# Performance work log

Measured on AMD Instinct MI355X. Metric: run time of the kernel, lower is better.

The kernel has to match this reference:

```python
import jax, jax.numpy as jnp
import numpy as np

B, S, D, H = 2, 2048, 1024, 16
HD = D // H  # head_dim = 64

def setup_inputs() -> dict:
    key = jax.random.key(0)
    ks = jax.random.split(key, 10)
    s = 1.0 / np.sqrt(D)
    return {
        "hidden_states": jax.random.normal(ks[0], (B, S, D), jnp.float32),
        "attention_mask": jnp.ones((B, S), jnp.float32),
        "q_w": jax.random.uniform(ks[1], (D, D), jnp.float32, -s, s),
        "q_b": jax.random.uniform(ks[2], (D,), jnp.float32, -s, s),
        "k_w": jax.random.uniform(ks[3], (D, D), jnp.float32, -s, s),
        "k_b": jax.random.uniform(ks[4], (D,), jnp.float32, -s, s),
        "v_w": jax.random.uniform(ks[5], (D, D), jnp.float32, -s, s),
        "v_b": jax.random.uniform(ks[6], (D,), jnp.float32, -s, s),
        "o_w": jax.random.uniform(ks[7], (D, D), jnp.float32, -s, s),
        "o_b": jax.random.uniform(ks[8], (D,), jnp.float32, -s, s),
    }

def reference(hidden_states, attention_mask, q_w, q_b, k_w, k_b, v_w, v_b, o_w, o_b):
    scale = HD ** -0.5
    # projections; torch Linear: x @ W^T + b. Here weights stored as (D, D) used directly.
    q = hidden_states @ q_w + q_b  # [B,S,D]
    k = hidden_states @ k_w + k_b
    v = hidden_states @ v_w + v_b
    # split heads -> [B,H,S,HD]
    q = q.reshape(B, S, H, HD).transpose(0, 2, 1, 3)
    k = k.reshape(B, S, H, HD).transpose(0, 2, 1, 3)
    v = v.reshape(B, S, H, HD).transpose(0, 2, 1, 3)
    scores = jnp.einsum('bhqd,bhkd->bhqk', q, k) * scale  # [B,H,S,S]
    # additive mask from 2D [B,S] mask (1=keep, 0=mask)
    scores = scores + (1.0 - attention_mask)[:, None, None, :] * -10000.0
    attn = jax.nn.softmax(scores, axis=-1)
    ctx = jnp.einsum('bhqk,bhkd->bhqd', attn, v)  # [B,H,S,HD]
    ctx = ctx.transpose(0, 2, 1, 3).reshape(B, S, D)
    return ctx @ o_w + o_b
```

## Files before the change

kernel.cpp:

```cpp
#include <hip/hip_runtime.h>
#include <hip/hip_bf16.h>

#define B_ 2
#define S_ 2048
#define D_ 1024
#define H_ 16
#define HD_ 64

#define QSCALE 0.18033688f
#define MLOG2E 14426.950408f

#define EXP2(x) __builtin_amdgcn_exp2f(x)

typedef __attribute__((ext_vector_type(8))) short bf16x8;
typedef __attribute__((ext_vector_type(4))) short short4v;
typedef __attribute__((ext_vector_type(4))) float floatx4;
typedef __attribute__((ext_vector_type(16))) float f32x16;

static __device__ __forceinline__ short f2bf(float f) {
  union { float f; unsigned int i; } c; c.f = f;
  unsigned int r = c.i + 0x7FFFu + ((c.i >> 16) & 1u);
  return (short)(r >> 16);
}

static __device__ __forceinline__ int cvtpk_bf16(float a, float b) {
  int r;
  asm("v_cvt_pk_bf16_f32 %0, %1, %2" : "=v"(r) : "v"(a), "v"(b));
  return r;
}
static __device__ __forceinline__ void swap32(int& a, int& b) {
  asm("v_permlane32_swap_b32 %0, %1" : "+v"(a), "+v"(b));
}

static __device__ __forceinline__ void gld_lds16(const void* g, void* l) {
  __builtin_amdgcn_global_load_lds(
      (const __attribute__((address_space(1))) unsigned int*)g,
      (__attribute__((address_space(3))) unsigned int*)l, 16, 0, 0);
}

__global__ __launch_bounds__(256)
void prep(const float* __restrict__ w0, const float* __restrict__ w1,
          const float* __restrict__ w2, const float* __restrict__ w3,
          const float* __restrict__ hs, short* __restrict__ WT,
          short* __restrict__ Xb) {
  const int z = blockIdx.z;
  if (z < 4) {
    __shared__ short t[64][65];
    const float* src = z == 0 ? w0 : z == 1 ? w1 : z == 2 ? w2 : w3;
    short* dst = WT + (size_t)z * D_ * D_;
    const int tx = threadIdx.x & 63, ty = threadIdx.x >> 6;
    const int r0 = blockIdx.y * 64, c0 = blockIdx.x * 64;
    for (int r = ty; r < 64; r += 4)
      t[r][tx] = f2bf(src[(size_t)(r0 + r) * D_ + c0 + tx]);
    __syncthreads();
    for (int r = ty; r < 64; r += 4)
      dst[(size_t)(c0 + r) * D_ + r0 + tx] = t[tx][r];
  } else {
    const int bid = blockIdx.y * 16 + blockIdx.x;
    const float4* in4 = (const float4*)hs;
    short4v* out4 = (short4v*)Xb;
#pragma unroll
    for (int i = 0; i < 16; i++) {
      const int idx = bid * 4096 + i * 256 + threadIdx.x;
      const float4 v = in4[idx];
      short4v o;
      o[0] = f2bf(v.x); o[1] = f2bf(v.y); o[2] = f2bf(v.z); o[3] = f2bf(v.w);
      out4[idx] = o;
    }
  }
}

__global__ __launch_bounds__(256, 2)
void gemm_qkv(const short* __restrict__ X, const short* __restrict__ WT,
              const float* __restrict__ qb, const float* __restrict__ kb,
              const float* __restrict__ vb,
              short* __restrict__ Qo, short* __restrict__ Ko,
              short* __restrict__ Vt) {
  __shared__ __align__(16) short As[128 * 32];
  __shared__ __align__(16) short Bs[128 * 32];
  const int tid = threadIdx.x;
  const int wave = tid >> 6, lane = tid & 63;
  const int col = lane & 15, quad = lane >> 4;
  const int m0 = blockIdx.x * 128;
  const int nt = blockIdx.y;
  const int widx = nt >> 3;
  const int n1 = (nt & 7) * 128;
  const short* Bsrc = WT + (size_t)widx * D_ * D_ + (size_t)n1 * D_;
  const int b = m0 >> 11;

  const int srow = tid >> 2;
  const int skcol = (tid & 3) * 8;
  const short* ga = X + (size_t)(m0 + srow) * D_ + skcol;
  const short* gb = Bsrc + (size_t)srow * D_ + skcol;
  short* la = As + tid * 8;
  short* lb = Bs + tid * 8;

  floatx4 acc[4][4];
#pragma unroll
  for (int i = 0; i < 4; i++)
#pragma unroll
    for (int j = 0; j < 4; j++) acc[i][j] = floatx4{0.f, 0.f, 0.f, 0.f};

  if (widx < 2) {
    const int wseq = (wave >> 1) * 64;
    const int wfeat = (wave & 1) * 64;
    for (int k0 = 0; k0 < D_; k0 += 32) {
      gld_lds16(ga, la);
      gld_lds16(ga + 64 * D_, la + 2048);
      gld_lds16(gb, lb);
      gld_lds16(gb + 64 * D_, lb + 2048);
      ga += 32; gb += 32;
      __syncthreads();
      bf16x8 xf[4], wf[4];
#pragma unroll
      for (int j = 0; j < 4; j++)
        xf[j] = *(const bf16x8*)(As + (wseq + j * 16 + col) * 32 + quad * 8);
#pragma unroll
      for (int i = 0; i < 4; i++)
        wf[i] = *(const bf16x8*)(Bs + (wfeat + i * 16 + col) * 32 + quad * 8);
#pragma unroll
      for (int i = 0; i < 4; i++)
#pragma unroll
        for (int j = 0; j < 4; j++)
          acc[i][j] = __builtin_amdgcn_mfma_f32_16x16x32_bf16(wf[i], xf[j],
                                                              acc[i][j], 0, 0, 0);
      __syncthreads();
    }
    const float* bias = widx == 0 ? qb : kb;
    short* dst = widx == 0 ? Qo : Ko;
    const float scale = widx == 0 ? QSCALE : 1.0f;
#pragma unroll
    for (int i = 0; i < 4; i++) {
      const int nf = n1 + wfeat + i * 16 + quad * 4;
      const int h = nf >> 6, hd = nf & 63;
      const float4 bv = *(const float4*)(bias + nf);
#pragma unroll
      for (int j = 0; j < 4; j++) {
        const int s = (m0 + wseq + j * 16 + col) & (S_ - 1);
        short4v pk;
        pk[0] = f2bf((acc[i][j][0] + bv.x) * scale);
        pk[1] = f2bf((acc[i][j][1] + bv.y) * scale);
        pk[2] = f2bf((acc[i][j][2] + bv.z) * scale);
        pk[3] = f2bf((acc[i][j][3] + bv.w) * scale);
        *(short4v*)(dst + ((size_t)(b * H_ + h) * S_ + s) * HD_ + hd) = pk;
      }
    }
  } else {
    const int wrow = (wave & 1) * 64;
    const int wcol = (wave >> 1) * 64;
    for (int k0 = 0; k0 < D_; k0 += 32) {
      gld_lds16(ga, la);
      gld_lds16(ga + 64 * D_, la + 2048);
      gld_lds16(gb, lb);
      gld_lds16(gb + 64 * D_, lb + 2048);
      ga += 32; gb += 32;
      __syncthreads();
      bf16x8 af[4], bfr[4];
#pragma unroll
      for (int i = 0; i < 4; i++)
        af[i] = *(const bf16x8*)(As + (wrow + i * 16 + col) * 32 + quad * 8);
#pragma unroll
      for (int j = 0; j < 4; j++)
        bfr[j] = *(const bf16x8*)(Bs + (wcol + j * 16 + col) * 32 + quad * 8);
#pragma unroll
      for (int i = 0; i < 4; i++)
#pragma unroll
        for (int j = 0; j < 4; j++)
          acc[i][j] = __builtin_amdgcn_mfma_f32_16x16x32_bf16(af[i], bfr[j],
                                                              acc[i][j], 0, 0, 0);
      __syncthreads();
    }
    float bv[4];
#pragma unroll
    for (int j = 0; j < 4; j++) bv[j] = vb[n1 + wcol + j * 16 + col];
#pragma unroll
    for (int i = 0; i < 4; i++) {
      const int s = (m0 + wrow + i * 16 + quad * 4) & (S_ - 1);
#pragma unroll
      for (int j = 0; j < 4; j++) {
        const int nl = n1 + wcol + j * 16 + col;
        const int h = nl >> 6, hd = nl & 63;
        short4v pk;
#pragma unroll
        for (int r = 0; r < 4; r++) pk[r] = f2bf(acc[i][j][r] + bv[j]);
        *(short4v*)(Vt + ((size_t)(b * H_ + h) * HD_ + hd) * S_ + s) = pk;
      }
    }
  }
}

__global__ __launch_bounds__(256, 2)
void attn(const short* __restrict__ Q, const short* __restrict__ K,
          const short* __restrict__ Vt, const float* __restrict__ mask,
          short* __restrict__ ctx) {
  __shared__ __align__(16) short Ks[2][8192];
  __shared__ __align__(16) short Vs[2][8192];
  __shared__ __align__(16) float Wb[S_];
  const int tid = threadIdx.x, wave = tid >> 6, lane = tid & 63;
  const int l31 = lane & 31, hi = lane >> 5, x7 = l31 & 7;
  const int lin = blockIdx.x;
  const int qt = (lin >> 3) & 15;
  const int gi = (lin & 7) + ((lin >> 7) << 3);
  const int h = gi & 15, b = gi >> 4;
  const short* Qh = Q + (size_t)(b * H_ + h) * S_ * HD_;
  const short* Kh = K + (size_t)(b * H_ + h) * S_ * HD_;
  const short* Vh = Vt + (size_t)(b * H_ + h) * HD_ * S_;
  const float* mk = mask + (size_t)b * S_;
  const int q0 = qt * 128 + wave * 32;

  int srow[4], schk[4], sts[4];
#pragma unroll
  for (int i = 0; i < 4; i++) {
    const int s = tid + i * 256;
    sts[i] = s >> 9;
    const int s9 = s & 511;
    srow[i] = s9 >> 3;
    schk[i] = ((s9 & 7) ^ (srow[i] & 7)) * 8;
  }

#pragma unroll
  for (int i = 0; i < 4; i++) {
    gld_lds16(Kh + (size_t)(sts[i] * 64 + srow[i]) * HD_ + schk[i],
              &Ks[0][(tid + i * 256) * 8]);
    gld_lds16(Vh + (size_t)srow[i] * S_ + sts[i] * 64 + schk[i],
              &Vs[0][(tid + i * 256) * 8]);
  }

  for (int i = tid; i < S_; i += 256)
    Wb[i] = (mk[i] - 1.0f) * MLOG2E;

  bf16x8 qf[4];
  {
    const short* qp = Qh + (size_t)(q0 + l31) * HD_ + hi * 8;
#pragma unroll
    for (int c = 0; c < 4; c++) qf[c] = *(const bf16x8*)(qp + c * 16);
  }

  bf16x8 ones;
#pragma unroll
  for (int i = 0; i < 8; i++) ones[i] = (short)0x3F80;

  f32x16 acc0, acc1, rsa;
#pragma unroll
  for (int r = 0; r < 16; r++) { acc0[r] = 0.f; acc1[r] = 0.f; rsa[r] = 0.f; }

  const int kbase = l31 * 64;
  int ko[4];
#pragma unroll
  for (int c = 0; c < 4; c++) ko[c] = ((((c << 1) | hi) ^ x7) << 3);

  __syncthreads();

  for (int it = 0; it < S_ / 128; it++) {
    const int buf = it & 1;
    const int kt = it * 128;
    if (it + 1 < S_ / 128) {
      const int kn = kt + 128;
#pragma unroll
      for (int i = 0; i < 4; i++) {
        gld_lds16(Kh + (size_t)(kn + sts[i] * 64 + srow[i]) * HD_ + schk[i],
                  &Ks[buf ^ 1][(tid + i * 256) * 8]);
        gld_lds16(Vh + (size_t)srow[i] * S_ + kn + sts[i] * 64 + schk[i],
                  &Vs[buf ^ 1][(tid + i * 256) * 8]);
      }
    }

#pragma unroll
    for (int t2 = 0; t2 < 2; t2++) {
      const int sub = t2 * 4096;
      const int ktt = kt + t2 * 64;

      bf16x8 pB[4];
#pragma unroll
      for (int t = 0; t < 2; t++) {
        const int kb2 = ktt + t * 32 + 4 * hi;
        const float4 b0 = *(const float4*)&Wb[kb2];
        const float4 b1 = *(const float4*)&Wb[kb2 + 8];
        const float4 b2 = *(const float4*)&Wb[kb2 + 16];
        const float4 b3 = *(const float4*)&Wb[kb2 + 24];
        f32x16 z;
        z[0] = b0.x; z[1] = b0.y; z[2]  = b0.z; z[3]  = b0.w;
        z[4] = b1.x; z[5] = b1.y; z[6]  = b1.z; z[7]  = b1.w;
        z[8] = b2.x; z[9] = b2.y; z[10] = b2.z; z[11] = b2.w;
        z[12] = b3.x; z[13] = b3.y; z[14] = b3.z; z[15] = b3.w;
        const short* kp = &Ks[buf][sub + t * 2048 + kbase];
        __builtin_amdgcn_s_setprio(1);
#pragma unroll
        for (int c = 0; c < 4; c++) {
          const bf16x8 kf = *(const bf16x8*)(kp + ko[c]);
          z = __builtin_amdgcn_mfma_f32_32x32x16_bf16(kf, qf[c], z, 0, 0, 0);
        }
        __builtin_amdgcn_s_setprio(0);
        float p[16];
#pragma unroll
        for (int r = 0; r < 16; r++) p[r] = EXP2(z[r]);
        int a0 = cvtpk_bf16(p[0], p[1]),   a1 = cvtpk_bf16(p[2], p[3]);
        int cc0 = cvtpk_bf16(p[4], p[5]),  cc1 = cvtpk_bf16(p[6], p[7]);
        int e0 = cvtpk_bf16(p[8], p[9]),   e1 = cvtpk_bf16(p[10], p[11]);
        int g0 = cvtpk_bf16(p[12], p[13]), g1 = cvtpk_bf16(p[14], p[15]);
        swap32(a0, cc0); swap32(a1, cc1);
        swap32(e0, g0);  swap32(e1, g1);
        union { int i[4]; bf16x8 v; } u0, u1;
        u0.i[0] = a0; u0.i[1] = a1; u0.i[2] = cc0; u0.i[3] = cc1;
        u1.i[0] = e0; u1.i[1] = e1; u1.i[2] = g0;  u1.i[3] = g1;
        pB[t * 2] = u0.v;
        pB[t * 2 + 1] = u1.v;
      }

      const short* vp0 = &Vs[buf][sub + kbase];
      const short* vp1 = &Vs[buf][sub + 2048 + kbase];
      __builtin_amdgcn_s_setprio(1);
#pragma unroll
      for (int kc = 0; kc < 4; kc++)
        rsa = __builtin_amdgcn_mfma_f32_32x32x16_bf16(ones, pB[kc], rsa, 0, 0, 0);
#pragma unroll
      for (int kc = 0; kc < 4; kc++) {
        const bf16x8 vf0 = *(const bf16x8*)(vp0 + ko[kc]);
        const bf16x8 vf1 = *(const bf16x8*)(vp1 + ko[kc]);
        acc0 = __builtin_amdgcn_mfma_f32_32x32x16_bf16(vf0, pB[kc], acc0, 0, 0, 0);
        acc1 = __builtin_amdgcn_mfma_f32_32x32x16_bf16(vf1, pB[kc], acc1, 0, 0, 0);
      }
      __builtin_amdgcn_s_setprio(0);
    }
    __syncthreads();
  }

  const float inv = 1.0f / (rsa[0] + 1e-30f);
  const size_t row = (size_t)b * S_ + q0 + l31;
#pragma unroll
  for (int g4 = 0; g4 < 4; g4++) {
    short4v o0, o1;
#pragma unroll
    for (int j = 0; j < 4; j++) {
      o0[j] = f2bf(acc0[g4 * 4 + j] * inv);
      o1[j] = f2bf(acc1[g4 * 4 + j] * inv);
    }
    short* cp = ctx + row * D_ + h * HD_ + g4 * 8 + 4 * hi;
    *(short4v*)(cp) = o0;
    *(short4v*)(cp + 32) = o1;
  }
}

__global__ __launch_bounds__(256, 2)
void gemm_out(const short* __restrict__ X, const short* __restrict__ WT,
              const float* __restrict__ ob, float* __restrict__ out) {
  __shared__ __align__(16) short As[64 * 32];
  __shared__ __align__(16) short Bs[128 * 32];
  const int tid = threadIdx.x;
  const int wave = tid >> 6, lane = tid & 63;
  const int col = lane & 15, quad = lane >> 4;
  const int m0 = blockIdx.x * 64;
  const int n0 = blockIdx.y * 128;
  const short* Bsrc = WT + (size_t)n0 * D_;
  const int wrow = (wave & 1) * 32;
  const int wcol = (wave >> 1) * 64;

  floatx4 acc[2][4];
#pragma unroll
  for (int i = 0; i < 2; i++)
#pragma unroll
    for (int j = 0; j < 4; j++) acc[i][j] = floatx4{0.f, 0.f, 0.f, 0.f};

  const int arow = tid >> 2, akcol = (tid & 3) * 8;
  const short* ga = X + (size_t)(m0 + arow) * D_ + akcol;
  const short* gb = Bsrc + (size_t)arow * D_ + akcol;
  short* la = As + tid * 8;
  short* lb = Bs + tid * 8;

  for (int k0 = 0; k0 < D_; k0 += 32) {
    gld_lds16(ga, la);
    gld_lds16(gb, lb);
    gld_lds16(gb + 64 * D_, lb + 2048);
    ga += 32; gb += 32;
    __syncthreads();
    bf16x8 af[2], bfr[4];
#pragma unroll
    for (int i = 0; i < 2; i++)
      af[i] = *(const bf16x8*)(As + (wrow + i * 16 + col) * 32 + quad * 8);
#pragma unroll
    for (int j = 0; j < 4; j++)
      bfr[j] = *(const bf16x8*)(Bs + (wcol + j * 16 + col) * 32 + quad * 8);
#pragma unroll
    for (int i = 0; i < 2; i++)
#pragma unroll
      for (int j = 0; j < 4; j++)
        acc[i][j] = __builtin_amdgcn_mfma_f32_16x16x32_bf16(af[i], bfr[j],
                                                            acc[i][j], 0, 0, 0);
    __syncthreads();
  }

  float bv[4];
#pragma unroll
  for (int j = 0; j < 4; j++) bv[j] = ob[n0 + wcol + j * 16 + col];

#pragma unroll
  for (int i = 0; i < 2; i++) {
    const int m = m0 + wrow + i * 16 + quad * 4;
#pragma unroll
    for (int j = 0; j < 4; j++) {
      const int n = n0 + wcol + j * 16 + col;
#pragma unroll
      for (int r = 0; r < 4; r++)
        out[(size_t)(m + r) * D_ + n] = acc[i][j][r] + bv[j];
    }
  }
}

extern "C" void kernel_launch(void* const* d_in, const int* in_sizes, int n_in,
                              void* d_out, int out_size, void* d_ws, size_t ws_size,
                              hipStream_t stream) {
  (void)in_sizes; (void)n_in; (void)out_size; (void)ws_size;
  const float* hs  = (const float*)d_in[0];
  const float* msk = (const float*)d_in[1];
  const float* qw  = (const float*)d_in[2];
  const float* qb  = (const float*)d_in[3];
  const float* kw  = (const float*)d_in[4];
  const float* kb  = (const float*)d_in[5];
  const float* vw  = (const float*)d_in[6];
  const float* vb  = (const float*)d_in[7];
  const float* ow  = (const float*)d_in[8];
  const float* ob  = (const float*)d_in[9];
  float* out = (float*)d_out;
  char* ws = (char*)d_ws;

  short* Xb  = (short*)(ws);
  short* WT  = (short*)(ws + (8ull  << 20));
  short* Qp  = (short*)(ws + (16ull << 20));
  short* Kp  = (short*)(ws + (24ull << 20));
  short* Vtp = (short*)(ws + (32ull << 20));
  short* Ctx = Xb;

  prep<<<dim3(16, 16, 5), 256, 0, stream>>>(qw, kw, vw, ow, hs, WT, Xb);
  gemm_qkv<<<dim3(32, 24), 256, 0, stream>>>(Xb, WT, qb, kb, vb, Qp, Kp, Vtp);
  attn<<<dim3(512), 256, 0, stream>>>(Qp, Kp, Vtp, msk, Ctx);
  gemm_out<<<dim3(64, 8), 256, 0, stream>>>(Ctx, WT + 3ull * D_ * D_, ob, out);
}
```

Baseline: 190.5 us.

## Double-buffer LDS with K=64 tiles and XOR swizzle in QKV and output GEMMs

Both projection GEMMs now use two LDS buffers with 64-wide K tiles. The next tile is issued via global-to-LDS loads before computing on the current one, so each iteration needs one barrier instead of two. An XOR swizzle on the 16-byte chunks spreads fragment reads across LDS banks. The change quadruples LDS per block (64 KB for the QKV GEMM), which may cut occupancy below the two blocks per CU the launch bounds request.

```diff
diff --git a/kernel.cpp b/kernel.cpp
--- a/kernel.cpp
+++ b/kernel.cpp
@@ -76,8 +76,8 @@
               const float* __restrict__ vb,
               short* __restrict__ Qo, short* __restrict__ Ko,
               short* __restrict__ Vt) {
-  __shared__ __align__(16) short As[128 * 32];
-  __shared__ __align__(16) short Bs[128 * 32];
+  __shared__ __align__(16) short As[2][8192];
+  __shared__ __align__(16) short Bs[2][8192];
   const int tid = threadIdx.x;
   const int wave = tid >> 6, lane = tid & 63;
   const int col = lane & 15, quad = lane >> 4;
@@ -88,42 +88,65 @@
   const short* Bsrc = WT + (size_t)widx * D_ * D_ + (size_t)n1 * D_;
   const int b = m0 >> 11;
 
-  const int srow = tid >> 2;
-  const int skcol = (tid & 3) * 8;
-  const short* ga = X + (size_t)(m0 + srow) * D_ + skcol;
-  const short* gb = Bsrc + (size_t)srow * D_ + skcol;
-  short* la = As + tid * 8;
-  short* lb = Bs + tid * 8;
+  int srow[4], schk[4];
+#pragma unroll
+  for (int i = 0; i < 4; i++) {
+    const int s = tid + i * 256;
+    srow[i] = s >> 3;
+    schk[i] = ((s & 7) ^ (srow[i] & 7)) * 8;
+  }
+
+#pragma unroll
+  for (int i = 0; i < 4; i++) {
+    gld_lds16(X + (size_t)(m0 + srow[i]) * D_ + schk[i],
+              &As[0][(tid + i * 256) * 8]);
+    gld_lds16(Bsrc + (size_t)srow[i] * D_ + schk[i],
+              &Bs[0][(tid + i * 256) * 8]);
+  }
 
   floatx4 acc[4][4];
 #pragma unroll
   for (int i = 0; i < 4; i++)
 #pragma unroll
     for (int j = 0; j < 4; j++) acc[i][j] = floatx4{0.f, 0.f, 0.f, 0.f};
+
+  const int sx0 = ((quad ^ (col & 7)) << 3);
+  const int sx1 = (((4 | quad) ^ (col & 7)) << 3);
+
+  __syncthreads();
 
   if (widx < 2) {
     const int wseq = (wave >> 1) * 64;
     const int wfeat = (wave & 1) * 64;
-    for (int k0 = 0; k0 < D_; k0 += 32) {
-      gld_lds16(ga, la);
-      gld_lds16(ga + 64 * D_, la + 2048);
-      gld_lds16(gb, lb);
-      gld_lds16(gb + 64 * D_, lb + 2048);
-      ga += 32; gb += 32;
-      __syncthreads();
-      bf16x8 xf[4], wf[4];
-#pragma unroll
-      for (int j = 0; j < 4; j++)
-        xf[j] = *(const bf16x8*)(As + (wseq + j * 16 + col) * 32 + quad * 8);
-#pragma unroll
-      for (int i = 0; i < 4; i++)
-        wf[i] = *(const bf16x8*)(Bs + (wfeat + i * 16 + col) * 32 + quad * 8);
-#pragma unroll
-      for (int i = 0; i < 4; i++)
+    for (int it = 0; it < 16; it++) {
+      const int buf = it & 1;
+      if (it + 1 < 16) {
+        const int k0 = (it + 1) * 64;
+#pragma unroll
+        for (int i = 0; i < 4; i++) {
+          gld_lds16(X + (size_t)(m0 + srow[i]) * D_ + k0 + schk[i],
+                    &As[buf ^ 1][(tid + i * 256) * 8]);
+          gld_lds16(Bsrc + (size_t)srow[i] * D_ + k0 + schk[i],
+                    &Bs[buf ^ 1][(tid + i * 256) * 8]);
+        }
+      }
+#pragma unroll
+      for (int kk = 0; kk < 2; kk++) {
+        const int sx = kk ? sx1 : sx0;
+        bf16x8 xf[4], wf[4];
 #pragma unroll
         for (int j = 0; j < 4; j++)
-          acc[i][j] = __builtin_amdgcn_mfma_f32_16x16x32_bf16(wf[i], xf[j],
-                                                              acc[i][j], 0, 0, 0);
+          xf[j] = *(const bf16x8*)(&As[buf][(wseq + j * 16 + col) * 64 + sx]);
+#pragma unroll
+        for (int i = 0; i < 4; i++)
+          wf[i] = *(const bf16x8*)(&Bs[buf][(wfeat + i * 16 + col) * 64 + sx]);
+#pragma unroll
+        for (int i = 0; i < 4; i++)
+#pragma unroll
+          for (int j = 0; j < 4; j++)
+            acc[i][j] = __builtin_amdgcn_mfma_f32_16x16x32_bf16(wf[i], xf[j],
+                                                                acc[i][j], 0, 0, 0);
+      }
       __syncthreads();
     }
     const float* bias = widx == 0 ? qb : kb;
@@ -148,26 +171,35 @@
   } else {
     const int wrow = (wave & 1) * 64;
     const int wcol = (wave >> 1) * 64;
-    for (int k0 = 0; k0 < D_; k0 += 32) {
-      gld_lds16(ga, la);
-      gld_lds16(ga + 64 * D_, la + 2048);
-      gld_lds16(gb, lb);
-      gld_lds16(gb + 64 * D_, lb + 2048);
-      ga += 32; gb += 32;
-      __syncthreads();
-      bf16x8 af[4], bfr[4];
-#pragma unroll
-      for (int i = 0; i < 4; i++)
-        af[i] = *(const bf16x8*)(As + (wrow + i * 16 + col) * 32 + quad * 8);
-#pragma unroll
-      for (int j = 0; j < 4; j++)
-        bfr[j] = *(const bf16x8*)(Bs + (wcol + j * 16 + col) * 32 + quad * 8);
-#pragma unroll
-      for (int i = 0; i < 4; i++)
+    for (int it = 0; it < 16; it++) {
+      const int buf = it & 1;
+      if (it + 1 < 16) {
+        const int k0 = (it + 1) * 64;
+#pragma unroll
+        for (int i = 0; i < 4; i++) {
+          gld_lds16(X + (size_t)(m0 + srow[i]) * D_ + k0 + schk[i],
+                    &As[buf ^ 1][(tid + i * 256) * 8]);
+          gld_lds16(Bsrc + (size_t)srow[i] * D_ + k0 + schk[i],
+                    &Bs[buf ^ 1][(tid + i * 256) * 8]);
+        }
+      }
+#pragma unroll
+      for (int kk = 0; kk < 2; kk++) {
+        const int sx = kk ? sx1 : sx0;
+        bf16x8 af[4], bfr[4];
+#pragma unroll
+        for (int i = 0; i < 4; i++)
+          af[i] = *(const bf16x8*)(&As[buf][(wrow + i * 16 + col) * 64 + sx]);
 #pragma unroll
         for (int j = 0; j < 4; j++)
-          acc[i][j] = __builtin_amdgcn_mfma_f32_16x16x32_bf16(af[i], bfr[j],
-                                                              acc[i][j], 0, 0, 0);
+          bfr[j] = *(const bf16x8*)(&Bs[buf][(wcol + j * 16 + col) * 64 + sx]);
+#pragma unroll
+        for (int i = 0; i < 4; i++)
+#pragma unroll
+          for (int j = 0; j < 4; j++)
+            acc[i][j] = __builtin_amdgcn_mfma_f32_16x16x32_bf16(af[i], bfr[j],
+                                                                acc[i][j], 0, 0, 0);
+      }
       __syncthreads();
     }
     float bv[4];
@@ -344,8 +376,8 @@
 __global__ __launch_bounds__(256, 2)
 void gemm_out(const short* __restrict__ X, const short* __restrict__ WT,
               const float* __restrict__ ob, float* __restrict__ out) {
-  __shared__ __align__(16) short As[64 * 32];
-  __shared__ __align__(16) short Bs[128 * 32];
+  __shared__ __align__(16) short As[2][4096];
+  __shared__ __align__(16) short Bs[2][8192];
   const int tid = threadIdx.x;
   const int wave = tid >> 6, lane = tid & 63;
   const int col = lane & 15, quad = lane >> 4;
@@ -355,37 +387,64 @@
   const int wrow = (wave & 1) * 32;
   const int wcol = (wave >> 1) * 64;
 
+  int srow[4], schk[4];
+#pragma unroll
+  for (int i = 0; i < 4; i++) {
+    const int s = tid + i * 256;
+    srow[i] = s >> 3;
+    schk[i] = ((s & 7) ^ (srow[i] & 7)) * 8;
+  }
+
+#pragma unroll
+  for (int i = 0; i < 2; i++)
+    gld_lds16(X + (size_t)(m0 + srow[i]) * D_ + schk[i],
+              &As[0][(tid + i * 256) * 8]);
+#pragma unroll
+  for (int i = 0; i < 4; i++)
+    gld_lds16(Bsrc + (size_t)srow[i] * D_ + schk[i],
+              &Bs[0][(tid + i * 256) * 8]);
+
   floatx4 acc[2][4];
 #pragma unroll
   for (int i = 0; i < 2; i++)
 #pragma unroll
     for (int j = 0; j < 4; j++) acc[i][j] = floatx4{0.f, 0.f, 0.f, 0.f};
 
-  const int arow = tid >> 2, akcol = (tid & 3) * 8;
-  const short* ga = X + (size_t)(m0 + arow) * D_ + akcol;
-  const short* gb = Bsrc + (size_t)arow * D_ + akcol;
-  short* la = As + tid * 8;
-  short* lb = Bs + tid * 8;
-
-  for (int k0 = 0; k0 < D_; k0 += 32) {
-    gld_lds16(ga, la);
-    gld_lds16(gb, lb);
-    gld_lds16(gb + 64 * D_, lb + 2048);
-    ga += 32; gb += 32;
-    __syncthreads();
-    bf16x8 af[2], bfr[4];
-#pragma unroll
-    for (int i = 0; i < 2; i++)
-      af[i] = *(const bf16x8*)(As + (wrow + i * 16 + col) * 32 + quad * 8);
-#pragma unroll
-    for (int j = 0; j < 4; j++)
-      bfr[j] = *(const bf16x8*)(Bs + (wcol + j * 16 + col) * 32 + quad * 8);
-#pragma unroll
-    for (int i = 0; i < 2; i++)
+  const int sx0 = ((quad ^ (col & 7)) << 3);
+  const int sx1 = (((4 | quad) ^ (col & 7)) << 3);
+
+  __syncthreads();
+
+  for (int it = 0; it < 16; it++) {
+    const int buf = it & 1;
+    if (it + 1 < 16) {
+      const int k0 = (it + 1) * 64;
+#pragma unroll
+      for (int i = 0; i < 2; i++)
+        gld_lds16(X + (size_t)(m0 + srow[i]) * D_ + k0 + schk[i],
+                  &As[buf ^ 1][(tid + i * 256) * 8]);
+#pragma unroll
+      for (int i = 0; i < 4; i++)
+        gld_lds16(Bsrc + (size_t)srow[i] * D_ + k0 + schk[i],
+                  &Bs[buf ^ 1][(tid + i * 256) * 8]);
+    }
+#pragma unroll
+    for (int kk = 0; kk < 2; kk++) {
+      const int sx = kk ? sx1 : sx0;
+      bf16x8 af[2], bfr[4];
+#pragma unroll
+      for (int i = 0; i < 2; i++)
+        af[i] = *(const bf16x8*)(&As[buf][(wrow + i * 16 + col) * 64 + sx]);
 #pragma unroll
       for (int j = 0; j < 4; j++)
-        acc[i][j] = __builtin_amdgcn_mfma_f32_16x16x32_bf16(af[i], bfr[j],
-                                                            acc[i][j], 0, 0, 0);
+        bfr[j] = *(const bf16x8*)(&Bs[buf][(wcol + j * 16 + col) * 64 + sx]);
+#pragma unroll
+      for (int i = 0; i < 2; i++)
+#pragma unroll
+        for (int j = 0; j < 4; j++)
+          acc[i][j] = __builtin_amdgcn_mfma_f32_16x16x32_bf16(af[i], bfr[j],
+                                                              acc[i][j], 0, 0, 0);
+    }
     __syncthreads();
   }
 
```

Result: slower. 195.0 us (+2.3%).
